# Optimization experiments

Hardware: AMD Instinct MI355X
Metric: run time of the kernel (lower is better)

## Reference

```python
import jax, jax.numpy as jnp
import numpy as np

N_NODES = 100000
N_EDGES = 1200000
N_GRAPHS = 512


def _init_linear(key, fan_in, fan_out):
    kw, kb = jax.random.split(key)
    lim = 1.0 / np.sqrt(fan_in)
    W = jax.random.uniform(kw, (fan_in, fan_out), minval=-lim, maxval=lim, dtype=jnp.float32)
    b = jax.random.uniform(kb, (fan_out,), minval=-lim, maxval=lim, dtype=jnp.float32)
    return W, b


def setup_inputs() -> dict:
    key = jax.random.key(0)
    ks = jax.random.split(key, 12)
    x = jax.random.normal(ks[0], (N_NODES, 10), dtype=jnp.float32)
    edge_index = jax.random.randint(ks[1], (2, N_EDGES), 0, N_NODES, dtype=jnp.int64)
    batch = jnp.sort(jax.random.randint(ks[2], (N_NODES,), 0, N_GRAPHS, dtype=jnp.int64))
    edge_weights = jax.random.uniform(ks[3], (N_EDGES,), dtype=jnp.float32)
    W1, b1 = _init_linear(ks[4], 10, 60)
    W2, b2 = _init_linear(ks[5], 60, 60)
    W3, b3 = _init_linear(ks[6], 60, 60)
    W4, b4 = _init_linear(ks[7], 60, 60)
    L1w, L1b = _init_linear(ks[8], 60, 60)
    L2w, L2b = _init_linear(ks[9], 60, 10)
    L3w, L3b = _init_linear(ks[10], 10, 2)
    return dict(x=x, edge_index=edge_index, batch=batch, edge_weights=edge_weights,
                W1=W1, b1=b1, W2=W2, b2=b2, W3=W3, b3=b3, W4=W4, b4=b4,
                L1w=L1w, L1b=L1b, L2w=L2w, L2b=L2b, L3w=L3w, L3b=L3b)


def gcn_conv(x, W, b, src, dst, ew, n):
    # PyG GCNConv: add self-loops (weight 1), symmetric normalization, linear, scatter-add.
    deg = jax.ops.segment_sum(ew, dst, num_segments=n) + 1.0  # +1 self-loop
    dinv = jnp.where(deg > 0, jax.lax.rsqrt(deg), 0.0)
    h = x @ W  # [n, out]
    norm = dinv[src] * ew * dinv[dst]  # [E]
    agg = jax.ops.segment_sum(h[src] * norm[:, None], dst, num_segments=n)
    agg = agg + h * (dinv * dinv)[:, None]  # self-loop contribution (weight 1)
    return agg + b


def _forward(x, edge_index, batch, edge_weights,
             W1, b1, W2, b2, W3, b3, W4, b4,
             L1w, L1b, L2w, L2b, L3w, L3b):
    src, dst = edge_index[0], edge_index[1]
    n = x.shape[0]
    h = jax.nn.relu(gcn_conv(x, W1, b1, src, dst, edge_weights, n))
    h = jax.nn.relu(gcn_conv(h, W2, b2, src, dst, edge_weights, n))
    h = jax.nn.relu(gcn_conv(h, W3, b3, src, dst, edge_weights, n))
    h = jax.nn.relu(gcn_conv(h, W4, b4, src, dst, edge_weights, n))
    g = jax.ops.segment_max(h, batch, num_segments=N_GRAPHS)
    g = jnp.where(jnp.isfinite(g), g, 0.0)  # guard empty graphs
    g = jax.nn.relu(g @ L1w + L1b)
    g = jax.nn.relu(g @ L2w + L2b)
    return g @ L3w + L3b


def reference(x, edge_index, batch, edge_weights,
              W1, b1, W2, b2, W3, b3, W4, b4,
              L1w, L1b, L2w, L2b, L3w, L3b):
    return _forward(x, edge_index, batch, edge_weights,
                    W1, b1, W2, b2, W3, b3, W4, b4,
                    L1w, L1b, L2w, L2b, L3w, L3b)
```

## Files before the change

kernel.cpp:

```cpp
#include <hip/hip_runtime.h>
#include <hip/hip_fp16.h>

#define N_NODES 100000
#define N_EDGES 1200000
#define N_GRAPHS 512
#define F 60
#define NPW 8
#define CAP 48
#define NBKT 782
#define EPB 4096
#define CPX 37
#define NCH 296
#define BKT_CAP 2048
#define WSC 3.0518509e-05f

__global__ void __launch_bounds__(256) k_hist(const int* __restrict__ dst,
                                              int* __restrict__ histM, int E) {
    __shared__ int h[NBKT];
    int c = (blockIdx.x & 7) * CPX + (blockIdx.x >> 3);
    for (int i = threadIdx.x; i < NBKT; i += 256) h[i] = 0;
    __syncthreads();
    int b0 = c * EPB;
    for (int i = threadIdx.x; i < EPB; i += 256) {
        int e = b0 + i;
        if (e < E) atomicAdd(&h[dst[e] >> 7], 1);
    }
    __syncthreads();
    for (int i = threadIdx.x; i < NBKT; i += 256) histM[c * NBKT + i] = h[i];
}

__global__ void k_scan_gstart(int* __restrict__ histM, int* __restrict__ tot,
                              const int* __restrict__ batch, int* __restrict__ gst, int n) {
    int bi = blockIdx.x;
    if (bi < 4) {
        int b = bi * 256 + threadIdx.x;
        if (b >= NBKT) return;
        int running = 0;
        for (int c = 0; c < NCH; c += 8) {
            int i0 = (c + 0) * NBKT + b, i1 = (c + 1) * NBKT + b;
            int i2 = (c + 2) * NBKT + b, i3 = (c + 3) * NBKT + b;
            int i4 = (c + 4) * NBKT + b, i5 = (c + 5) * NBKT + b;
            int i6 = (c + 6) * NBKT + b, i7 = (c + 7) * NBKT + b;
            int v0 = histM[i0], v1 = histM[i1], v2 = histM[i2], v3 = histM[i3];
            int v4 = histM[i4], v5 = histM[i5], v6 = histM[i6], v7 = histM[i7];
            histM[i0] = running; running += v0;
            histM[i1] = running; running += v1;
            histM[i2] = running; running += v2;
            histM[i3] = running; running += v3;
            histM[i4] = running; running += v4;
            histM[i5] = running; running += v5;
            histM[i6] = running; running += v6;
            histM[i7] = running; running += v7;
        }
        tot[b] = running;
    } else {
        int i = (bi - 4) * 256 + threadIdx.x;
        if (i >= n) return;
        int b = batch[i];
        int pb = (i == 0) ? -1 : batch[i - 1];
        for (int g = pb + 1; g <= b; ++g) gst[g] = i;
        if (i == n - 1) for (int g = b + 1; g <= N_GRAPHS; ++g) gst[g] = n;
    }
}

__global__ void __launch_bounds__(256) k_fill(const int* __restrict__ src,
                                              const int* __restrict__ dst,
                                              const float* __restrict__ ew,
                                              const int* __restrict__ histM,
                                              int2* __restrict__ bkt, int E) {
    __shared__ int h[NBKT];
    int c = (blockIdx.x & 7) * CPX + (blockIdx.x >> 3);
    for (int i = threadIdx.x; i < NBKT; i += 256) h[i] = 0;
    __syncthreads();
    int b0 = c * EPB;
    const int* bas = histM + c * NBKT;
    for (int i = threadIdx.x; i < EPB; i += 256) {
        int e = b0 + i;
        if (e >= E) continue;
        int d = dst[e];
        int b = d >> 7;
        int r = atomicAdd(&h[b], 1);
        int pos = bas[b] + r;
        if (pos < BKT_CAP) {
            int2 p;
            p.x = src[e] | ((d & 127) << 17);
            p.y = __float_as_int(ew[e]);
            bkt[(size_t)b * BKT_CAP + pos] = p;
        }
    }
}

__global__ void __launch_bounds__(256) k_build(
        const int* __restrict__ tot, const int2* __restrict__ bkt,
        unsigned* __restrict__ csr, int* __restrict__ cnt,
        float* __restrict__ dinv, const float* __restrict__ x,
        float* __restrict__ xs, int n) {
    __shared__ int lcur[128];
    __shared__ float ldeg[128];
    int b = blockIdx.x, tid = threadIdx.x;
    if (tid < 128) { lcur[tid] = 0; ldeg[tid] = 0.f; }
    __syncthreads();
    int nbase = b << 7;
    int m = min(tot[b], BKT_CAP);
    const int2* sb = bkt + (size_t)b * BKT_CAP;
    for (int i = tid; i < m; i += 256) {
        int2 p = sb[i];
        int srcv = p.x & 0x1FFFF;
        int low = (p.x >> 17) & 127;
        int pos = atomicAdd(&lcur[low], 1);
        if (pos < CAP) {
            unsigned w15 = (unsigned)(int)rintf(__int_as_float(p.y) * 32767.f);
            csr[(size_t)(nbase + low) * CAP + pos] = (unsigned)srcv | (w15 << 17);
        }
        atomicAdd(&ldeg[low], __int_as_float(p.y));
    }
    __syncthreads();
    if (tid < 128) {
        int v = nbase + tid;
        if (v < n) {
            int mA = min(lcur[tid], CAP);
            cnt[v] = mA;
            float di = rsqrtf(ldeg[tid] + 1.0f);
            dinv[v] = di;
            #pragma unroll
            for (int c2 = 0; c2 < 10; ++c2) xs[v * 16 + c2] = di * x[v * 10 + c2];
            #pragma unroll
            for (int c2 = 10; c2 < 16; ++c2) xs[v * 16 + c2] = 0.f;
            int g0 = tid & ~7;
            int m8 = 0;
            #pragma unroll
            for (int i2 = 0; i2 < 8; ++i2) m8 = max(m8, min(lcur[g0 + i2], CAP));
            int R = (m8 + 3) & ~3;
            for (int e = mA; e < R; ++e) csr[(size_t)v * CAP + e] = 0u;
        }
    }
}

template<bool FIRST, bool SCALE_OUT>
__global__ void __launch_bounds__(256) k_layer(
        const void* __restrict__ HinV, const float* __restrict__ W,
        const float* __restrict__ bias,
        const unsigned* __restrict__ csr, const int* __restrict__ cnt,
        const float* __restrict__ dinv,
        __half* __restrict__ Hout, int n) {
    constexpr int WIN = FIRST ? 10 : 60;
    constexpr int WINP = FIRST ? 12 : 60;
    const float*  Hf = (const float*)HinV;
    const __half* Hh = (const __half*)HinV;
    __shared__ float Ws[WINP * 64];
    __shared__ __align__(16) float accS[4][NPW][64];
    for (int i = threadIdx.x; i < WINP * 64; i += 256) {
        int k = i >> 6, j = i & 63;
        Ws[i] = (j < F && k < WIN) ? W[k * F + j] : 0.f;
    }

    int wave = threadIdx.x >> 6;
    int lane = threadIdx.x & 63;
    float bj = (lane < F) ? bias[lane] : 0.f;
    int base = (blockIdx.x * 4 + wave) * NPW;

    if constexpr (FIRST) {
        __syncthreads();
        int l16 = lane & 15;
        int q = lane >> 4;
        #pragma unroll
        for (int p = 0; p < 2; ++p) {
            int v = base + 4 * p + q;
            float a = Hf[v * 16 + l16];
            int mm = cnt[v];
            int t1 = max(mm, __shfl_xor(mm, 16));
            int mu = max(t1, __shfl_xor(t1, 32));
            const unsigned* seg = csr + (size_t)v * CAP;
            for (int e = 0; e < mu; e += 4) {
                uint4 qq = *(const uint4*)(seg + e);
                float x0 = Hf[(qq.x & 0x1FFFF) * 16 + l16];
                float x1 = Hf[(qq.y & 0x1FFFF) * 16 + l16];
                float x2 = Hf[(qq.z & 0x1FFFF) * 16 + l16];
                float x3 = Hf[(qq.w & 0x1FFFF) * 16 + l16];
                a = fmaf((float)(qq.x >> 17) * WSC, x0, a);
                a = fmaf((float)(qq.y >> 17) * WSC, x1, a);
                a = fmaf((float)(qq.z >> 17) * WSC, x2, a);
                a = fmaf((float)(qq.w >> 17) * WSC, x3, a);
            }
            accS[wave][4 * p + q][l16] = a * dinv[v];
        }
        float o[NPW];
        #pragma unroll
        for (int t = 0; t < NPW; ++t) o[t] = bj;
        const float4* aq = (const float4*)&accS[wave][0][0];
        #pragma unroll
        for (int kq = 0; kq < 3; ++kq) {
            float w0 = Ws[(4 * kq + 0) * 64 + lane];
            float w1 = Ws[(4 * kq + 1) * 64 + lane];
            float w2 = Ws[(4 * kq + 2) * 64 + lane];
            float w3 = Ws[(4 * kq + 3) * 64 + lane];
            #pragma unroll
            for (int t = 0; t < NPW; ++t) {
                float4 aa = aq[t * 16 + kq];
                o[t] = fmaf(aa.x, w0, o[t]);
                o[t] = fmaf(aa.y, w1, o[t]);
                o[t] = fmaf(aa.z, w2, o[t]);
                o[t] = fmaf(aa.w, w3, o[t]);
            }
        }
        #pragma unroll
        for (int t = 0; t < NPW; ++t) {
            float sc = SCALE_OUT ? dinv[base + t] : 1.f;
            Hout[(size_t)(base + t) * 64 + lane] = __float2half_rn(fmaxf(o[t], 0.f) * sc);
        }
    } else {
        __syncthreads();
        int h  = lane >> 5;
        int lh = lane & 31;
        int fo = lh * 2;

        float2 acc2[4];
        float dis[4];
        const unsigned* seg[4];
        #pragma unroll
        for (int p = 0; p < 4; ++p) {
            int v = base + 2 * p + h;
            dis[p] = dinv[v];
            __half2 sh = *(const __half2*)(Hh + (size_t)v * 64 + fo);
            acc2[p].x = __low2float(sh);
            acc2[p].y = __high2float(sh);
            seg[p] = csr + (size_t)v * CAP;
        }
        int cmy = cnt[base + (lane & 7)];
        int m1 = max(cmy, __shfl_xor(cmy, 1));
        int m2 = max(m1, __shfl_xor(m1, 2));
        int mu = max(m2, __shfl_xor(m2, 4));

        for (int e = 0; e < mu; e += 4) {
            uint4 q[4];
            #pragma unroll
            for (int p = 0; p < 4; ++p) q[p] = *(const uint4*)(seg[p] + e);
            #pragma unroll
            for (int p = 0; p < 4; ++p) {
                unsigned e0 = q[p].x, e1 = q[p].y, e2 = q[p].z, e3 = q[p].w;
                __half2 g0 = *(const __half2*)(Hh + (size_t)(e0 & 0x1FFFF) * 64 + fo);
                __half2 g1 = *(const __half2*)(Hh + (size_t)(e1 & 0x1FFFF) * 64 + fo);
                __half2 g2 = *(const __half2*)(Hh + (size_t)(e2 & 0x1FFFF) * 64 + fo);
                __half2 g3 = *(const __half2*)(Hh + (size_t)(e3 & 0x1FFFF) * 64 + fo);
                float w0 = (float)(e0 >> 17) * WSC;
                float w1 = (float)(e1 >> 17) * WSC;
                float w2 = (float)(e2 >> 17) * WSC;
                float w3 = (float)(e3 >> 17) * WSC;
                acc2[p].x = fmaf(w0, __low2float(g0), acc2[p].x);
                acc2[p].y = fmaf(w0, __high2float(g0), acc2[p].y);
                acc2[p].x = fmaf(w1, __low2float(g1), acc2[p].x);
                acc2[p].y = fmaf(w1, __high2float(g1), acc2[p].y);
                acc2[p].x = fmaf(w2, __low2float(g2), acc2[p].x);
                acc2[p].y = fmaf(w2, __high2float(g2), acc2[p].y);
                acc2[p].x = fmaf(w3, __low2float(g3), acc2[p].x);
                acc2[p].y = fmaf(w3, __high2float(g3), acc2[p].y);
            }
        }
        #pragma unroll
        for (int p = 0; p < 4; ++p) {
            acc2[p].x *= dis[p]; acc2[p].y *= dis[p];
            *(float2*)&accS[wave][2 * p + h][fo] = acc2[p];
        }

        float o[NPW];
        #pragma unroll
        for (int t = 0; t < NPW; ++t) o[t] = bj;
        const float4* aq = (const float4*)&accS[wave][0][0];
        #pragma unroll
        for (int kq = 0; kq < 15; ++kq) {
            float w0 = Ws[(4 * kq + 0) * 64 + lane];
            float w1 = Ws[(4 * kq + 1) * 64 + lane];
            float w2 = Ws[(4 * kq + 2) * 64 + lane];
            float w3 = Ws[(4 * kq + 3) * 64 + lane];
            #pragma unroll
            for (int t = 0; t < NPW; ++t) {
                float4 aa = aq[t * 16 + kq];
                o[t] = fmaf(aa.x, w0, o[t]);
                o[t] = fmaf(aa.y, w1, o[t]);
                o[t] = fmaf(aa.z, w2, o[t]);
                o[t] = fmaf(aa.w, w3, o[t]);
            }
        }
        #pragma unroll
        for (int t = 0; t < NPW; ++t) {
            float sc = SCALE_OUT ? dinv[base + t] : 1.f;
            Hout[(size_t)(base + t) * 64 + lane] = __float2half_rn(fmaxf(o[t], 0.f) * sc);
        }
    }
}

__global__ void __launch_bounds__(256) k_poolmlp(
        const __half* __restrict__ H, const int* __restrict__ start,
        const float* __restrict__ L1w, const float* __restrict__ L1b,
        const float* __restrict__ L2w, const float* __restrict__ L2b,
        const float* __restrict__ L3w, const float* __restrict__ L3b,
        float* __restrict__ out) {
    __shared__ float red[4 * F];
    __shared__ float gin[F], h1[F], h2[10];
    int gi = blockIdx.x;
    int wave = threadIdx.x >> 6;
    int lane = threadIdx.x & 63;
    int t = threadIdx.x;
    int s = start[gi], e = start[gi + 1];
    float m = 0.f;
    for (int i = s + wave; i < e; i += 4)
        m = fmaxf(m, __half2float(H[(size_t)i * 64 + lane]));
    if (lane < F) red[wave * F + lane] = m;
    __syncthreads();
    if (t < F)
        gin[t] = fmaxf(fmaxf(red[t], red[F + t]), fmaxf(red[2 * F + t], red[3 * F + t]));
    __syncthreads();
    if (t < F) {
        float a = L1b[t];
        for (int k = 0; k < F; ++k) a += gin[k] * L1w[k * F + t];
        h1[t] = fmaxf(a, 0.f);
    }
    __syncthreads();
    if (t < 10) {
        float a = L2b[t];
        for (int k = 0; k < F; ++k) a += h1[k] * L2w[k * 10 + t];
        h2[t] = fmaxf(a, 0.f);
    }
    __syncthreads();
    if (t < 2) {
        float a = L3b[t];
        for (int k = 0; k < 10; ++k) a += h2[k] * L3w[k * 2 + t];
        out[gi * 2 + t] = a;
    }
}

extern "C" void kernel_launch(void* const* d_in, const int* in_sizes, int n_in,
                              void* d_out, int out_size, void* d_ws, size_t ws_size,
                              hipStream_t stream) {
    const int n = N_NODES, E = N_EDGES;
    const float* x   = (const float*)d_in[0];
    const int* ei    = (const int*)d_in[1];
    const int* batch = (const int*)d_in[2];
    const float* ew  = (const float*)d_in[3];
    const float* W1 = (const float*)d_in[4],  *b1 = (const float*)d_in[5];
    const float* W2 = (const float*)d_in[6],  *b2 = (const float*)d_in[7];
    const float* W3 = (const float*)d_in[8],  *b3 = (const float*)d_in[9];
    const float* W4 = (const float*)d_in[10], *b4 = (const float*)d_in[11];
    const float* L1w = (const float*)d_in[12], *L1b = (const float*)d_in[13];
    const float* L2w = (const float*)d_in[14], *L2b = (const float*)d_in[15];
    const float* L3w = (const float*)d_in[16], *L3b = (const float*)d_in[17];
    float* out = (float*)d_out;

    const int* src = ei;
    const int* dst = ei + E;

    char* ws = (char*)d_ws;
    size_t off = 0;
    auto carve = [&](size_t bytes) {
        void* p = ws + off;
        off += (bytes + 255) & ~size_t(255);
        return p;
    };
    int*      cnt   = (int*)carve(n * 4);
    float*    dinv  = (float*)carve(n * 4);
    int*      gst   = (int*)carve((N_GRAPHS + 1) * 4);
    unsigned* csr   = (unsigned*)carve((size_t)n * CAP * 4);
    int2*     bkt   = (int2*)carve((size_t)NBKT * BKT_CAP * 8);
    int*      histM = (int*)carve((size_t)NCH * NBKT * 4);
    int*      tot   = (int*)carve(NBKT * 4);
    float*    xs    = (float*)carve((size_t)n * 16 * 4);
    __half*   hA    = (__half*)carve((size_t)n * 64 * 2);
    __half*   hB    = (__half*)carve((size_t)n * 64 * 2);
    (void)ws_size;

    const int NB = (n + 255) / 256;
    const int LB = n / (4 * NPW);

    k_hist<<<NCH, 256, 0, stream>>>(dst, histM, E);
    k_scan_gstart<<<4 + NB, 256, 0, stream>>>(histM, tot, batch, gst, n);
    k_fill<<<NCH, 256, 0, stream>>>(src, dst, ew, histM, bkt, E);
    k_build<<<NBKT, 256, 0, stream>>>(tot, bkt, csr, cnt, dinv, x, xs, n);

    k_layer<true,  true ><<<LB, 256, 0, stream>>>(xs, W1, b1, csr, cnt, dinv, hA, n);
    k_layer<false, true ><<<LB, 256, 0, stream>>>(hA, W2, b2, csr, cnt, dinv, hB, n);
    k_layer<false, true ><<<LB, 256, 0, stream>>>(hB, W3, b3, csr, cnt, dinv, hA, n);
    k_layer<false, false><<<LB, 256, 0, stream>>>(hA, W4, b4, csr, cnt, dinv, hB, n);

    k_poolmlp<<<N_GRAPHS, 256, 0, stream>>>(hB, gst, L1w, L1b, L2w, L2b, L3w, L3b, out);
}
```

Baseline: 228.3 us.

## Interleave CSR edge slots across 8-node groups and precompute per-group loop bound

Changes the padded CSR from per-node rows to an 8-node interleaved layout, so each 4-edge chunk for a whole wave's group of 8 nodes sits in one contiguous 128-byte block. The build kernel also stores the rounded maximum edge count per group, which replaces the per-node counts and the shuffle reduction in the layer kernels. The first layer now processes both node halves in one loop instead of two. The goal is more coalesced index loads and fewer instructions per layer, at the cost of more complex indexing and scattered writes during the build.

After: 223.1 us, median of 2. 1.02x faster.

```diff
diff --git a/kernel.cpp b/kernel.cpp
--- a/kernel.cpp
+++ b/kernel.cpp
@@ -7,6 +7,7 @@
 #define F 60
 #define NPW 8
 #define CAP 48
+#define GSTRIDE 384
 #define NBKT 782
 #define EPB 4096
 #define CPX 37
@@ -92,7 +93,7 @@
 
 __global__ void __launch_bounds__(256) k_build(
         const int* __restrict__ tot, const int2* __restrict__ bkt,
-        unsigned* __restrict__ csr, int* __restrict__ cnt,
+        unsigned* __restrict__ csr, int* __restrict__ rnd,
         float* __restrict__ dinv, const float* __restrict__ x,
         float* __restrict__ xs, int n) {
     __shared__ int lcur[128];
@@ -110,7 +111,9 @@
         int pos = atomicAdd(&lcur[low], 1);
         if (pos < CAP) {
             unsigned w15 = (unsigned)(int)rintf(__int_as_float(p.y) * 32767.f);
-            csr[(size_t)(nbase + low) * CAP + pos] = (unsigned)srcv | (w15 << 17);
+            int v = nbase + low;
+            size_t idx = (size_t)(v >> 3) * GSTRIDE + (pos >> 2) * 32 + (v & 7) * 4 + (pos & 3);
+            csr[idx] = (unsigned)srcv | (w15 << 17);
         }
         atomicAdd(&ldeg[low], __int_as_float(p.y));
     }
@@ -119,7 +122,6 @@
         int v = nbase + tid;
         if (v < n) {
             int mA = min(lcur[tid], CAP);
-            cnt[v] = mA;
             float di = rsqrtf(ldeg[tid] + 1.0f);
             dinv[v] = di;
             #pragma unroll
@@ -131,7 +133,11 @@
             #pragma unroll
             for (int i2 = 0; i2 < 8; ++i2) m8 = max(m8, min(lcur[g0 + i2], CAP));
             int R = (m8 + 3) & ~3;
-            for (int e = mA; e < R; ++e) csr[(size_t)v * CAP + e] = 0u;
+            size_t gb = (size_t)(v >> 3) * GSTRIDE;
+            int p8 = v & 7;
+            for (int e = mA; e < R; ++e)
+                csr[gb + (e >> 2) * 32 + p8 * 4 + (e & 3)] = 0u;
+            if ((tid & 7) == 0) rnd[v >> 3] = R;
         }
     }
 }
@@ -140,7 +146,7 @@
 __global__ void __launch_bounds__(256) k_layer(
         const void* __restrict__ HinV, const float* __restrict__ W,
         const float* __restrict__ bias,
-        const unsigned* __restrict__ csr, const int* __restrict__ cnt,
+        const unsigned* __restrict__ csr, const int* __restrict__ rnd,
         const float* __restrict__ dinv,
         __half* __restrict__ Hout, int n) {
     constexpr int WIN = FIRST ? 10 : 60;
@@ -158,32 +164,39 @@
     int lane = threadIdx.x & 63;
     float bj = (lane < F) ? bias[lane] : 0.f;
     int base = (blockIdx.x * 4 + wave) * NPW;
+    int g = base >> 3;
+    const unsigned* segG = csr + (size_t)g * GSTRIDE;
+    int mu = rnd[g];
 
     if constexpr (FIRST) {
         __syncthreads();
         int l16 = lane & 15;
-        int q = lane >> 4;
-        #pragma unroll
-        for (int p = 0; p < 2; ++p) {
-            int v = base + 4 * p + q;
-            float a = Hf[v * 16 + l16];
-            int mm = cnt[v];
-            int t1 = max(mm, __shfl_xor(mm, 16));
-            int mu = max(t1, __shfl_xor(t1, 32));
-            const unsigned* seg = csr + (size_t)v * CAP;
-            for (int e = 0; e < mu; e += 4) {
-                uint4 qq = *(const uint4*)(seg + e);
-                float x0 = Hf[(qq.x & 0x1FFFF) * 16 + l16];
-                float x1 = Hf[(qq.y & 0x1FFFF) * 16 + l16];
-                float x2 = Hf[(qq.z & 0x1FFFF) * 16 + l16];
-                float x3 = Hf[(qq.w & 0x1FFFF) * 16 + l16];
-                a = fmaf((float)(qq.x >> 17) * WSC, x0, a);
-                a = fmaf((float)(qq.y >> 17) * WSC, x1, a);
-                a = fmaf((float)(qq.z >> 17) * WSC, x2, a);
-                a = fmaf((float)(qq.w >> 17) * WSC, x3, a);
-            }
-            accS[wave][4 * p + q][l16] = a * dinv[v];
-        }
+        int qt = lane >> 4;
+        float a0 = Hf[(base + qt) * 16 + l16];
+        float a1 = Hf[(base + 4 + qt) * 16 + l16];
+        for (int e = 0; e < mu; e += 4) {
+            const unsigned* ch = segG + (e >> 2) * 32;
+            uint4 qa = *(const uint4*)(ch + qt * 4);
+            uint4 qb = *(const uint4*)(ch + (4 + qt) * 4);
+            float x0 = Hf[(qa.x & 0x1FFFF) * 16 + l16];
+            float x1 = Hf[(qa.y & 0x1FFFF) * 16 + l16];
+            float x2 = Hf[(qa.z & 0x1FFFF) * 16 + l16];
+            float x3 = Hf[(qa.w & 0x1FFFF) * 16 + l16];
+            float y0 = Hf[(qb.x & 0x1FFFF) * 16 + l16];
+            float y1 = Hf[(qb.y & 0x1FFFF) * 16 + l16];
+            float y2 = Hf[(qb.z & 0x1FFFF) * 16 + l16];
+            float y3 = Hf[(qb.w & 0x1FFFF) * 16 + l16];
+            a0 = fmaf((float)(qa.x >> 17) * WSC, x0, a0);
+            a0 = fmaf((float)(qa.y >> 17) * WSC, x1, a0);
+            a0 = fmaf((float)(qa.z >> 17) * WSC, x2, a0);
+            a0 = fmaf((float)(qa.w >> 17) * WSC, x3, a0);
+            a1 = fmaf((float)(qb.x >> 17) * WSC, y0, a1);
+            a1 = fmaf((float)(qb.y >> 17) * WSC, y1, a1);
+            a1 = fmaf((float)(qb.z >> 17) * WSC, y2, a1);
+            a1 = fmaf((float)(qb.w >> 17) * WSC, y3, a1);
+        }
+        accS[wave][qt][l16]     = a0 * dinv[base + qt];
+        accS[wave][4 + qt][l16] = a1 * dinv[base + 4 + qt];
         float o[NPW];
         #pragma unroll
         for (int t = 0; t < NPW; ++t) o[t] = bj;
@@ -216,7 +229,6 @@
 
         float2 acc2[4];
         float dis[4];
-        const unsigned* seg[4];
         #pragma unroll
         for (int p = 0; p < 4; ++p) {
             int v = base + 2 * p + h;
@@ -224,17 +236,13 @@
             __half2 sh = *(const __half2*)(Hh + (size_t)v * 64 + fo);
             acc2[p].x = __low2float(sh);
             acc2[p].y = __high2float(sh);
-            seg[p] = csr + (size_t)v * CAP;
-        }
-        int cmy = cnt[base + (lane & 7)];
-        int m1 = max(cmy, __shfl_xor(cmy, 1));
-        int m2 = max(m1, __shfl_xor(m1, 2));
-        int mu = max(m2, __shfl_xor(m2, 4));
+        }
 
         for (int e = 0; e < mu; e += 4) {
+            const unsigned* ch = segG + (e >> 2) * 32;
             uint4 q[4];
             #pragma unroll
-            for (int p = 0; p < 4; ++p) q[p] = *(const uint4*)(seg[p] + e);
+            for (int p = 0; p < 4; ++p) q[p] = *(const uint4*)(ch + (2 * p + h) * 4);
             #pragma unroll
             for (int p = 0; p < 4; ++p) {
                 unsigned e0 = q[p].x, e1 = q[p].y, e2 = q[p].z, e3 = q[p].w;
@@ -356,7 +364,7 @@
         off += (bytes + 255) & ~size_t(255);
         return p;
     };
-    int*      cnt   = (int*)carve(n * 4);
+    int*      rnd   = (int*)carve((n / 8) * 4);
     float*    dinv  = (float*)carve(n * 4);
     int*      gst   = (int*)carve((N_GRAPHS + 1) * 4);
     unsigned* csr   = (unsigned*)carve((size_t)n * CAP * 4);
@@ -374,12 +382,12 @@
     k_hist<<<NCH, 256, 0, stream>>>(dst, histM, E);
     k_scan_gstart<<<4 + NB, 256, 0, stream>>>(histM, tot, batch, gst, n);
     k_fill<<<NCH, 256, 0, stream>>>(src, dst, ew, histM, bkt, E);
-    k_build<<<NBKT, 256, 0, stream>>>(tot, bkt, csr, cnt, dinv, x, xs, n);
-
-    k_layer<true,  true ><<<LB, 256, 0, stream>>>(xs, W1, b1, csr, cnt, dinv, hA, n);
-    k_layer<false, true ><<<LB, 256, 0, stream>>>(hA, W2, b2, csr, cnt, dinv, hB, n);
-    k_layer<false, true ><<<LB, 256, 0, stream>>>(hB, W3, b3, csr, cnt, dinv, hA, n);
-    k_layer<false, false><<<LB, 256, 0, stream>>>(hA, W4, b4, csr, cnt, dinv, hB, n);
+    k_build<<<NBKT, 256, 0, stream>>>(tot, bkt, csr, rnd, dinv, x, xs, n);
+
+    k_layer<true,  true ><<<LB, 256, 0, stream>>>(xs, W1, b1, csr, rnd, dinv, hA, n);
+    k_layer<false, true ><<<LB, 256, 0, stream>>>(hA, W2, b2, csr, rnd, dinv, hB, n);
+    k_layer<false, true ><<<LB, 256, 0, stream>>>(hB, W3, b3, csr, rnd, dinv, hA, n);
+    k_layer<false, false><<<LB, 256, 0, stream>>>(hA, W4, b4, csr, rnd, dinv, hB, n);
 
     k_poolmlp<<<N_GRAPHS, 256, 0, stream>>>(hB, gst, L1w, L1b, L2w, L2b, L3w, L3b, out);
 }
```
